# Performance work log

Measured on AMD Instinct MI355X. Metric: run time of the kernel, lower is better.

## Reference

```python
import jax, jax.numpy as jnp
import numpy as np

N_NODES = 10000


def sage_conv(x, src, dst, W_l, b_l, W_r):
    # PyG SAGEConv with mean aggregation:
    #   out = lin_l(mean_{j in N(i)} x_j) + lin_r(x_i)
    msgs = x[src]  # [E, d] gather of source-node features
    agg = jax.ops.segment_sum(msgs, dst, num_segments=N_NODES)  # [N, d]
    cnt = jax.ops.segment_sum(jnp.ones((src.shape[0],), x.dtype), dst,
                              num_segments=N_NODES)  # [N]
    mean = agg / jnp.maximum(cnt, 1.0)[:, None]  # zero rows for isolated nodes
    return mean @ W_l + b_l + x @ W_r


def setup_inputs() -> dict:
    key = jax.random.key(0)
    ks = jax.random.split(key, 12)
    in_c, hid, out_c = 128, 128, 128
    x = jax.random.normal(ks[0], (N_NODES, in_c), dtype=jnp.float32)
    edge_index = jax.random.randint(ks[1], (2, 640000), 0, N_NODES, dtype=jnp.int64)

    def lin(k, fan_in, fan_out):
        s = 1.0 / np.sqrt(fan_in)
        return jax.random.uniform(k, (fan_in, fan_out), jnp.float32, -s, s)

    params = {
        'W1_l': lin(ks[2], in_c, hid), 'b1_l': jnp.zeros((hid,), jnp.float32),
        'W1_r': lin(ks[3], in_c, hid),
        'W2_l': lin(ks[4], hid, hid), 'b2_l': jnp.zeros((hid,), jnp.float32),
        'W2_r': lin(ks[5], hid, hid),
        'W3_l': lin(ks[6], hid, out_c), 'b3_l': jnp.zeros((out_c,), jnp.float32),
        'W3_r': lin(ks[7], hid, out_c),
        'W_cls': lin(ks[8], out_c, 1), 'b_cls': jnp.zeros((1,), jnp.float32),
    }
    return {'x': x, 'edge_index': edge_index, **params}


def reference(x, edge_index, W1_l, b1_l, W1_r, W2_l, b2_l, W2_r,
              W3_l, b3_l, W3_r, W_cls, b_cls):
    src, dst = edge_index[0], edge_index[1]
    h = jax.nn.relu(sage_conv(x, src, dst, W1_l, b1_l, W1_r))
    # dropout is identity in eval mode
    h = jax.nn.relu(sage_conv(h, src, dst, W2_l, b2_l, W2_r))
    h = jax.nn.relu(sage_conv(h, src, dst, W3_l, b3_l, W3_r))
    logits = h @ W_cls + b_cls  # [N, 1]
    return jax.nn.sigmoid(logits)[:, 0]  # [N]
```

## Files before the change

kernel.cpp:

```cpp
#include <hip/hip_runtime.h>
#include <hip/hip_fp16.h>
#include <math.h>

#define N_NODES 10000
#define D 128
#define NCOPY 16

typedef unsigned int uint_t;
typedef __attribute__((ext_vector_type(8))) _Float16 f16x8;
typedef __attribute__((ext_vector_type(4))) float f32x4;

#define MFMA16(a, b, c) __builtin_amdgcn_mfma_f32_16x16x32_f16((a), (b), (c), 0, 0, 0)

__device__ inline uint_t pack_h2(float lo, float hi) {
    __half2 h = __floats2half2_rn(lo, hi);
    return *(uint_t*)&h;
}
__device__ inline void acc_h8(uint4 v, float4& aA, float4& aB) {
    float2 f;
    f = __half22float2(*(__half2*)&v.x); aA.x += f.x; aA.y += f.y;
    f = __half22float2(*(__half2*)&v.y); aA.z += f.x; aA.w += f.y;
    f = __half22float2(*(__half2*)&v.z); aB.x += f.x; aB.y += f.y;
    f = __half22float2(*(__half2*)&v.w); aB.z += f.x; aB.w += f.y;
}

__global__ void prep_kernel(const float* __restrict__ x, __half* __restrict__ xm,
                            const float* __restrict__ W1l, const float* __restrict__ W1r,
                            const float* __restrict__ W2l, const float* __restrict__ W2r,
                            const float* __restrict__ W3l, const float* __restrict__ W3r,
                            __half* __restrict__ WT,
                            uint4* __restrict__ degz, int n8, int nz16, int nwt) {
    int i = blockIdx.x * blockDim.x + threadIdx.x;
    if (i < nz16) degz[i] = make_uint4(0u, 0u, 0u, 0u);
    if (i < n8) {
        const float4* p = (const float4*)x + (size_t)i * 2;
        float4 a = p[0], b = p[1];
        uint4 o;
        o.x = pack_h2(a.x, a.y); o.y = pack_h2(a.z, a.w);
        o.z = pack_h2(b.x, b.y); o.w = pack_h2(b.z, b.w);
        ((uint4*)xm)[i] = o;
    }
    if (i < nwt) {
        int m = i >> 14, idx = i & 16383;
        int n = idx >> 7, k = idx & 127;
        const float* Wm = (m == 0) ? W1l : (m == 1) ? W1r : (m == 2) ? W2l
                        : (m == 3) ? W2r : (m == 4) ? W3l : W3r;
        WT[i] = __float2half_rn(Wm[k * D + n]);
    }
}

__global__ void rank_kernel(const int* __restrict__ dst, int E,
                            int* __restrict__ degN, int* __restrict__ pos) {
    int i = blockIdx.x * blockDim.x + threadIdx.x;
    if (i < E) {
        int c = blockIdx.x & (NCOPY - 1);
        pos[i] = atomicAdd(&degN[c * N_NODES + dst[i]], 1);
    }
}

__global__ void sumdeg_kernel(const int* __restrict__ degN, int* __restrict__ tot, int n) {
    int i = blockIdx.x * blockDim.x + threadIdx.x;
    if (i < n) {
        int s = 0;
#pragma unroll
        for (int c = 0; c < NCOPY; ++c) s += degN[c * N_NODES + i];
        tot[i] = s;
    }
}

#define SCAN_PER 10
#define SCAN_N 10240
__global__ __launch_bounds__(1024) void scan_kernel(const int* __restrict__ tot,
                                                    int* __restrict__ offsets, int n) {
    __shared__ int buf[SCAN_N];
    __shared__ int wsum[16];
    __shared__ int wpre[16];
    int tid = threadIdx.x;
    int lane = tid & 63, wid = tid >> 6;
#pragma unroll
    for (int q = 0; q < SCAN_PER; ++q) {
        int idx = q * 1024 + tid;
        buf[idx] = (idx < n) ? tot[idx] : 0;
    }
    __syncthreads();
    int base = tid * SCAN_PER;
    int loc[SCAN_PER];
    int s = 0;
#pragma unroll
    for (int q = 0; q < SCAN_PER; ++q) {
        s += buf[base + q];
        loc[q] = s;
    }
    int mysum = s;
#pragma unroll
    for (int off = 1; off < 64; off <<= 1) {
        int t = __shfl_up(s, off, 64);
        if (lane >= off) s += t;
    }
    if (lane == 63) wsum[wid] = s;
    __syncthreads();
    if (wid == 0 && lane < 16) {
        int v = wsum[lane];
        int ss = v;
#pragma unroll
        for (int off = 1; off < 16; off <<= 1) {
            int t = __shfl_up(ss, off, 16);
            if ((lane & 15) >= off) ss += t;
        }
        wpre[lane] = ss - v;
    }
    __syncthreads();
    int thread_excl = wpre[wid] + (s - mysum);
#pragma unroll
    for (int q = 0; q < SCAN_PER; ++q) buf[base + q] = thread_excl + loc[q];
    __syncthreads();
#pragma unroll
    for (int q = 0; q < SCAN_PER; ++q) {
        int idx = q * 1024 + tid;
        if (idx < n) offsets[idx + 1] = buf[idx];
    }
    if (tid == 0) offsets[0] = 0;
}

__global__ void baseN_kernel(const int* __restrict__ degN, const int* __restrict__ offsets,
                             int* __restrict__ baseN, int n) {
    int i = blockIdx.x * blockDim.x + threadIdx.x;
    if (i < n) {
        int run = offsets[i];
#pragma unroll
        for (int c = 0; c < NCOPY; ++c) {
            baseN[c * N_NODES + i] = run;
            run += degN[c * N_NODES + i];
        }
    }
}

__global__ void csr_write_kernel(const int* __restrict__ src, const int* __restrict__ dst,
                                 const int* __restrict__ pos, int E,
                                 const int* __restrict__ baseN, int* __restrict__ csr_src) {
    int i = blockIdx.x * blockDim.x + threadIdx.x;
    if (i < E) {
        int c = (i >> 8) & (NCOPY - 1);
        csr_src[baseN[c * N_NODES + dst[i]] + pos[i]] = src[i];
    }
}

__global__ __launch_bounds__(256) void aggregate_kernel(const __half* __restrict__ h16,
                                                        const int* __restrict__ offsets,
                                                        const int* __restrict__ csr_src,
                                                        __half* __restrict__ mean16) {
    __shared__ float tmp[3][16][8];
    int node = blockIdx.x;
    int tid = threadIdx.x;
    int g = tid >> 4;
    int fl = tid & 15;
    int beg = offsets[node], end = offsets[node + 1];
    float4 aA = make_float4(0.f, 0.f, 0.f, 0.f);
    float4 aB = make_float4(0.f, 0.f, 0.f, 0.f);
    float4 cA = make_float4(0.f, 0.f, 0.f, 0.f);
    float4 cB = make_float4(0.f, 0.f, 0.f, 0.f);
    int e = beg + g;
    for (; e + 16 < end; e += 32) {
        int s0 = csr_src[e];
        int s1 = csr_src[e + 16];
        uint4 v0 = *(const uint4*)&h16[s0 * D + fl * 8];
        uint4 v1 = *(const uint4*)&h16[s1 * D + fl * 8];
        acc_h8(v0, aA, aB);
        acc_h8(v1, cA, cB);
    }
    if (e < end) {
        int s0 = csr_src[e];
        uint4 v0 = *(const uint4*)&h16[s0 * D + fl * 8];
        acc_h8(v0, aA, aB);
    }
    aA.x += cA.x; aA.y += cA.y; aA.z += cA.z; aA.w += cA.w;
    aB.x += cB.x; aB.y += cB.y; aB.z += cB.z; aB.w += cB.w;
    aA.x += __shfl_xor(aA.x, 16, 64); aA.y += __shfl_xor(aA.y, 16, 64);
    aA.z += __shfl_xor(aA.z, 16, 64); aA.w += __shfl_xor(aA.w, 16, 64);
    aB.x += __shfl_xor(aB.x, 16, 64); aB.y += __shfl_xor(aB.y, 16, 64);
    aB.z += __shfl_xor(aB.z, 16, 64); aB.w += __shfl_xor(aB.w, 16, 64);
    aA.x += __shfl_xor(aA.x, 32, 64); aA.y += __shfl_xor(aA.y, 32, 64);
    aA.z += __shfl_xor(aA.z, 32, 64); aA.w += __shfl_xor(aA.w, 32, 64);
    aB.x += __shfl_xor(aB.x, 32, 64); aB.y += __shfl_xor(aB.y, 32, 64);
    aB.z += __shfl_xor(aB.z, 32, 64); aB.w += __shfl_xor(aB.w, 32, 64);
    int wv = tid >> 6;
    int lane = tid & 63;
    if (wv > 0 && lane < 16) {
        *(float4*)&tmp[wv - 1][lane][0] = aA;
        *(float4*)&tmp[wv - 1][lane][4] = aB;
    }
    __syncthreads();
    if (tid < 16) {
#pragma unroll
        for (int w = 0; w < 3; ++w) {
            float4 oA = *(const float4*)&tmp[w][tid][0];
            float4 oB = *(const float4*)&tmp[w][tid][4];
            aA.x += oA.x; aA.y += oA.y; aA.z += oA.z; aA.w += oA.w;
            aB.x += oB.x; aB.y += oB.y; aB.z += oB.z; aB.w += oB.w;
        }
        int cnt = end - beg;
        float inv = (cnt > 0) ? (1.0f / (float)cnt) : 0.f;
        uint4 o;
        o.x = pack_h2(aA.x * inv, aA.y * inv);
        o.y = pack_h2(aA.z * inv, aA.w * inv);
        o.z = pack_h2(aB.x * inv, aB.y * inv);
        o.w = pack_h2(aB.z * inv, aB.w * inv);
        *(uint4*)&mean16[node * D + tid * 8] = o;
    }
}

__global__ __launch_bounds__(128) void lin_mfma_kernel(
        const __half* __restrict__ A1, const __half* __restrict__ A2,
        const __half* __restrict__ BT1, const __half* __restrict__ BT2,
        const float* __restrict__ bias, __half* __restrict__ out16,
        const float* __restrict__ Wc, const float* __restrict__ bcls,
        float* __restrict__ cls) {
    __shared__ float pl[2][16];
    int r0 = blockIdx.x * 16;
    int w  = (int)threadIdx.x >> 6;
    int l  = (int)threadIdx.x & 63;
    int lr = l & 15;
    int kg = l >> 4;

    const __half* a1p = A1 + (r0 + lr) * D + kg * 8;
    const __half* a2p = A2 + (r0 + lr) * D + kg * 8;
    f16x8 a1f[4], a2f[4];
#pragma unroll
    for (int ko = 0; ko < 4; ++ko) {
        a1f[ko] = *(const f16x8*)(a1p + ko * 32);
        a2f[ko] = *(const f16x8*)(a2p + ko * 32);
    }

    float p0 = 0.f, p1 = 0.f, p2 = 0.f, p3 = 0.f;

#pragma unroll
    for (int ct = 0; ct < 4; ++ct) {
        int c = w * 64 + ct * 16 + lr;
        const __half* b1p = BT1 + c * D + kg * 8;
        const __half* b2p = BT2 + c * D + kg * 8;
        f32x4 acc = {0.f, 0.f, 0.f, 0.f};
#pragma unroll
        for (int ko = 0; ko < 4; ++ko)
            acc = MFMA16(a1f[ko], *(const f16x8*)(b1p + ko * 32), acc);
#pragma unroll
        for (int ko = 0; ko < 4; ++ko)
            acc = MFMA16(a2f[ko], *(const f16x8*)(b2p + ko * 32), acc);

        float bcol = bias[c];
        float v0 = fmaxf(acc[0] + bcol, 0.f);
        float v1 = fmaxf(acc[1] + bcol, 0.f);
        float v2 = fmaxf(acc[2] + bcol, 0.f);
        float v3 = fmaxf(acc[3] + bcol, 0.f);
        if (Wc) {
            float wc = Wc[c];
            p0 += v0 * wc; p1 += v1 * wc; p2 += v2 * wc; p3 += v3 * wc;
        } else {
            int rbase = (r0 + kg * 4) * D + c;
            out16[rbase]         = __float2half_rn(v0);
            out16[rbase + D]     = __float2half_rn(v1);
            out16[rbase + 2 * D] = __float2half_rn(v2);
            out16[rbase + 3 * D] = __float2half_rn(v3);
        }
    }

    if (Wc) {
#pragma unroll
        for (int off = 1; off <= 8; off <<= 1) {
            p0 += __shfl_xor(p0, off, 64);
            p1 += __shfl_xor(p1, off, 64);
            p2 += __shfl_xor(p2, off, 64);
            p3 += __shfl_xor(p3, off, 64);
        }
        if (lr == 0) {
            pl[w][kg * 4 + 0] = p0;
            pl[w][kg * 4 + 1] = p1;
            pl[w][kg * 4 + 2] = p2;
            pl[w][kg * 4 + 3] = p3;
        }
        __syncthreads();
        if (threadIdx.x < 16) {
            float s = pl[0][threadIdx.x] + pl[1][threadIdx.x] + bcls[0];
            cls[r0 + threadIdx.x] = 1.0f / (1.0f + expf(-s));
        }
    }
}

extern "C" void kernel_launch(void* const* d_in, const int* in_sizes, int n_in,
                              void* d_out, int out_size, void* d_ws, size_t ws_size,
                              hipStream_t stream) {
    const float* x   = (const float*)d_in[0];
    const int* eidx  = (const int*)d_in[1];
    int E = in_sizes[1] / 2;
    const int* src = eidx;
    const int* dst = eidx + E;
    const float* W1l = (const float*)d_in[2];
    const float* b1  = (const float*)d_in[3];
    const float* W1r = (const float*)d_in[4];
    const float* W2l = (const float*)d_in[5];
    const float* b2  = (const float*)d_in[6];
    const float* W2r = (const float*)d_in[7];
    const float* W3l = (const float*)d_in[8];
    const float* b3  = (const float*)d_in[9];
    const float* W3r = (const float*)d_in[10];
    const float* Wc  = (const float*)d_in[11];
    const float* bc  = (const float*)d_in[12];
    float* out = (float*)d_out;

    char* p = (char*)d_ws;
    int* degN      = (int*)p;   p += (size_t)NCOPY * N_NODES * 4;
    int* baseN     = (int*)p;   p += (size_t)NCOPY * N_NODES * 4;
    int* offsets   = (int*)p;   p += 40960;
    int* tot       = (int*)p;   p += 40960;
    int* csr_src   = (int*)p;   p += (size_t)E * 4;
    int* pos       = (int*)p;   p += (size_t)E * 4;
    __half* mean16 = (__half*)p; p += (size_t)N_NODES * D * 2;
    __half* xm     = (__half*)p; p += (size_t)N_NODES * D * 2;
    __half* m1     = (__half*)p; p += (size_t)N_NODES * D * 2;
    __half* m2     = (__half*)p; p += (size_t)N_NODES * D * 2;
    __half* WT     = (__half*)p; p += (size_t)6 * D * D * 2;

    int n8  = N_NODES * D / 8;
    int nz16 = (NCOPY * N_NODES * 4) / 16;
    int nwt = 6 * D * D;
    prep_kernel<<<(n8 + 255) / 256, 256, 0, stream>>>(
        x, xm, W1l, W1r, W2l, W2r, W3l, W3r, WT, (uint4*)degN, n8, nz16, nwt);

    int eb = (E + 255) / 256;
    int nb = (N_NODES + 255) / 256;
    rank_kernel<<<eb, 256, 0, stream>>>(dst, E, degN, pos);
    sumdeg_kernel<<<nb, 256, 0, stream>>>(degN, tot, N_NODES);
    scan_kernel<<<1, 1024, 0, stream>>>(tot, offsets, N_NODES);
    baseN_kernel<<<nb, 256, 0, stream>>>(degN, offsets, baseN, N_NODES);
    csr_write_kernel<<<eb, 256, 0, stream>>>(src, dst, pos, E, baseN, csr_src);

    int lin_grid = N_NODES / 16;

    aggregate_kernel<<<N_NODES, 256, 0, stream>>>(xm, offsets, csr_src, mean16);
    lin_mfma_kernel<<<lin_grid, 128, 0, stream>>>(
        mean16, xm, WT, WT + D * D, b1, m1,
        (const float*)nullptr, (const float*)nullptr, (float*)nullptr);
    aggregate_kernel<<<N_NODES, 256, 0, stream>>>(m1, offsets, csr_src, mean16);
    lin_mfma_kernel<<<lin_grid, 128, 0, stream>>>(
        mean16, m1, WT + 2 * D * D, WT + 3 * D * D, b2, m2,
        (const float*)nullptr, (const float*)nullptr, (float*)nullptr);
    aggregate_kernel<<<N_NODES, 256, 0, stream>>>(m2, offsets, csr_src, mean16);
    lin_mfma_kernel<<<lin_grid, 128, 0, stream>>>(
        mean16, m2, WT + 4 * D * D, WT + 5 * D * D, b3, (__half*)nullptr,
        Wc, bc, out);
}
```

Baseline: 129.4 us.

## Replace global-atomic degree counting with per-block shared-memory histograms for CSR build

Edge ranking moves from global atomics over 16 replicated degree arrays to a per-block LDS histogram over contiguous chunks of 8192 edges, which are then written out as per-block histograms. This removes global atomic contention and the zeroing of the degree copies. In exchange only about 79 blocks run the histogram phase, leaving most CUs idle, and the sum and base kernels each loop over about 79 rows instead of 16, adding global traffic.

```diff
diff --git a/kernel.cpp b/kernel.cpp
--- a/kernel.cpp
+++ b/kernel.cpp
@@ -4,7 +4,8 @@
 
 #define N_NODES 10000
 #define D 128
-#define NCOPY 16
+#define PER_SHIFT 13
+#define PER (1 << PER_SHIFT)
 
 typedef unsigned int uint_t;
 typedef __attribute__((ext_vector_type(8))) _Float16 f16x8;
@@ -28,10 +29,8 @@
                             const float* __restrict__ W1l, const float* __restrict__ W1r,
                             const float* __restrict__ W2l, const float* __restrict__ W2r,
                             const float* __restrict__ W3l, const float* __restrict__ W3r,
-                            __half* __restrict__ WT,
-                            uint4* __restrict__ degz, int n8, int nz16, int nwt) {
+                            __half* __restrict__ WT, int n8, int nwt) {
     int i = blockIdx.x * blockDim.x + threadIdx.x;
-    if (i < nz16) degz[i] = make_uint4(0u, 0u, 0u, 0u);
     if (i < n8) {
         const float4* p = (const float4*)x + (size_t)i * 2;
         float4 a = p[0], b = p[1];
@@ -49,21 +48,28 @@
     }
 }
 
-__global__ void rank_kernel(const int* __restrict__ dst, int E,
-                            int* __restrict__ degN, int* __restrict__ pos) {
-    int i = blockIdx.x * blockDim.x + threadIdx.x;
-    if (i < E) {
-        int c = blockIdx.x & (NCOPY - 1);
-        pos[i] = atomicAdd(&degN[c * N_NODES + dst[i]], 1);
-    }
-}
-
-__global__ void sumdeg_kernel(const int* __restrict__ degN, int* __restrict__ tot, int n) {
+__global__ __launch_bounds__(256) void hist_kernel(const int* __restrict__ dst, int E,
+                                                   int* __restrict__ blockHist,
+                                                   int* __restrict__ pos) {
+    __shared__ int h[N_NODES];
+    int b = blockIdx.x;
+    for (int j = threadIdx.x; j < N_NODES; j += 256) h[j] = 0;
+    __syncthreads();
+    int beg = b << PER_SHIFT;
+    int end = min(beg + PER, E);
+    for (int i = beg + (int)threadIdx.x; i < end; i += 256)
+        pos[i] = atomicAdd(&h[dst[i]], 1);
+    __syncthreads();
+    int* bh = blockHist + (size_t)b * N_NODES;
+    for (int j = threadIdx.x; j < N_NODES; j += 256) bh[j] = h[j];
+}
+
+__global__ void sumNB_kernel(const int* __restrict__ blockHist, int NB,
+                             int* __restrict__ tot, int n) {
     int i = blockIdx.x * blockDim.x + threadIdx.x;
     if (i < n) {
         int s = 0;
-#pragma unroll
-        for (int c = 0; c < NCOPY; ++c) s += degN[c * N_NODES + i];
+        for (int b = 0; b < NB; ++b) s += blockHist[(size_t)b * N_NODES + i];
         tot[i] = s;
     }
 }
@@ -122,26 +128,26 @@
     if (tid == 0) offsets[0] = 0;
 }
 
-__global__ void baseN_kernel(const int* __restrict__ degN, const int* __restrict__ offsets,
-                             int* __restrict__ baseN, int n) {
+__global__ void baseNB_kernel(const int* __restrict__ blockHist,
+                              const int* __restrict__ offsets, int NB,
+                              int* __restrict__ baseB, int n) {
     int i = blockIdx.x * blockDim.x + threadIdx.x;
     if (i < n) {
         int run = offsets[i];
-#pragma unroll
-        for (int c = 0; c < NCOPY; ++c) {
-            baseN[c * N_NODES + i] = run;
-            run += degN[c * N_NODES + i];
+        for (int b = 0; b < NB; ++b) {
+            baseB[(size_t)b * N_NODES + i] = run;
+            run += blockHist[(size_t)b * N_NODES + i];
         }
     }
 }
 
 __global__ void csr_write_kernel(const int* __restrict__ src, const int* __restrict__ dst,
                                  const int* __restrict__ pos, int E,
-                                 const int* __restrict__ baseN, int* __restrict__ csr_src) {
+                                 const int* __restrict__ baseB, int* __restrict__ csr_src) {
     int i = blockIdx.x * blockDim.x + threadIdx.x;
     if (i < E) {
-        int c = (i >> 8) & (NCOPY - 1);
-        csr_src[baseN[c * N_NODES + dst[i]] + pos[i]] = src[i];
+        int b = i >> PER_SHIFT;
+        csr_src[baseB[(size_t)b * N_NODES + dst[i]] + pos[i]] = src[i];
     }
 }
 
@@ -306,9 +312,11 @@
     const float* bc  = (const float*)d_in[12];
     float* out = (float*)d_out;
 
+    int NB = (E + PER - 1) >> PER_SHIFT;
+
     char* p = (char*)d_ws;
-    int* degN      = (int*)p;   p += (size_t)NCOPY * N_NODES * 4;
-    int* baseN     = (int*)p;   p += (size_t)NCOPY * N_NODES * 4;
+    int* blockHist = (int*)p;   p += (size_t)NB * N_NODES * 4;
+    int* baseB     = (int*)p;   p += (size_t)NB * N_NODES * 4;
     int* offsets   = (int*)p;   p += 40960;
     int* tot       = (int*)p;   p += 40960;
     int* csr_src   = (int*)p;   p += (size_t)E * 4;
@@ -320,18 +328,17 @@
     __half* WT     = (__half*)p; p += (size_t)6 * D * D * 2;
 
     int n8  = N_NODES * D / 8;
-    int nz16 = (NCOPY * N_NODES * 4) / 16;
     int nwt = 6 * D * D;
     prep_kernel<<<(n8 + 255) / 256, 256, 0, stream>>>(
-        x, xm, W1l, W1r, W2l, W2r, W3l, W3r, WT, (uint4*)degN, n8, nz16, nwt);
+        x, xm, W1l, W1r, W2l, W2r, W3l, W3r, WT, n8, nwt);
 
     int eb = (E + 255) / 256;
     int nb = (N_NODES + 255) / 256;
-    rank_kernel<<<eb, 256, 0, stream>>>(dst, E, degN, pos);
-    sumdeg_kernel<<<nb, 256, 0, stream>>>(degN, tot, N_NODES);
+    hist_kernel<<<NB, 256, 0, stream>>>(dst, E, blockHist, pos);
+    sumNB_kernel<<<nb, 256, 0, stream>>>(blockHist, NB, tot, N_NODES);
     scan_kernel<<<1, 1024, 0, stream>>>(tot, offsets, N_NODES);
-    baseN_kernel<<<nb, 256, 0, stream>>>(degN, offsets, baseN, N_NODES);
-    csr_write_kernel<<<eb, 256, 0, stream>>>(src, dst, pos, E, baseN, csr_src);
+    baseNB_kernel<<<nb, 256, 0, stream>>>(blockHist, offsets, NB, baseB, N_NODES);
+    csr_write_kernel<<<eb, 256, 0, stream>>>(src, dst, pos, E, baseB, csr_src);
 
     int lin_grid = N_NODES / 16;
 
```

Result: slower. 137.8 us (+6.5%).
